# Kernel tuning notes

Hardware: AMD Instinct MI355X
Metric: run time of the kernel (lower is better)

The kernel has to match this reference:

```python
import jax, jax.numpy as jnp
import numpy as np

VOCAB = 10000
EMB = 512
CNN_FEAT = 2048
HID = 512
LAYERS = 2
BATCH = 128
SEQ = 32


def setup_inputs() -> dict:
    key = jax.random.key(0)
    ks = jax.random.split(key, 20)
    scale0 = 1.0 / np.sqrt(HID + EMB)
    scale1 = 1.0 / np.sqrt(HID + HID)
    inp = {
        "cnn_features": jax.random.normal(ks[0], (BATCH, CNN_FEAT), dtype=jnp.float32),
        "xTokens": jax.random.randint(ks[1], (BATCH, SEQ), 0, VOCAB),
        "embedding": jax.random.normal(ks[2], (VOCAB, EMB), dtype=jnp.float32),
        "in_W": jax.random.normal(ks[3], (CNN_FEAT, HID), dtype=jnp.float32) / np.sqrt(CNN_FEAT),
        "in_b": jnp.zeros((HID,), dtype=jnp.float32),
        # GRU layer 0 (input size EMB)
        "Wu0": jax.random.normal(ks[4], (EMB + HID, HID), dtype=jnp.float32) * scale0,
        "bu0": jnp.zeros((HID,), dtype=jnp.float32),
        "Wr0": jax.random.normal(ks[5], (EMB + HID, HID), dtype=jnp.float32) * scale0,
        "br0": jnp.zeros((HID,), dtype=jnp.float32),
        "Wc0": jax.random.normal(ks[6], (EMB + HID, HID), dtype=jnp.float32) * scale0,
        "bc0": jnp.zeros((HID,), dtype=jnp.float32),
        # GRU layer 1 (input size HID)
        "Wu1": jax.random.normal(ks[7], (HID + HID, HID), dtype=jnp.float32) * scale1,
        "bu1": jnp.zeros((HID,), dtype=jnp.float32),
        "Wr1": jax.random.normal(ks[8], (HID + HID, HID), dtype=jnp.float32) * scale1,
        "br1": jnp.zeros((HID,), dtype=jnp.float32),
        "Wc1": jax.random.normal(ks[9], (HID + HID, HID), dtype=jnp.float32) * scale1,
        "bc1": jnp.zeros((HID,), dtype=jnp.float32),
        "out_W": jax.random.normal(ks[10], (HID, VOCAB), dtype=jnp.float32) / np.sqrt(HID),
        "out_b": jnp.zeros((VOCAB,), dtype=jnp.float32),
    }
    return inp


def _gru(x, h, Wu, bu, Wr, br, Wc, bc):
    cat = jnp.concatenate([x, h], axis=1)                    # [B, in+H]
    u = jax.nn.sigmoid(cat @ Wu + bu)
    r = jax.nn.sigmoid(cat @ Wr + br)
    c = jnp.tanh(jnp.concatenate([x, r * h], axis=1) @ Wc + bc)
    return u * h + (1.0 - u) * c


def reference(cnn_features, xTokens, embedding, in_W, in_b,
              Wu0, bu0, Wr0, br0, Wc0, bc0,
              Wu1, bu1, Wr1, br1, Wc1, bc1,
              out_W, out_b):
    layer_params = [(Wu0, bu0, Wr0, br0, Wc0, bc0),
                    (Wu1, bu1, Wr1, br1, Wc1, bc1)]
    # initial hidden state from CNN features, replicated across layers
    h0 = jnp.tanh(cnn_features @ in_W + in_b)                # [B, H]
    init_state = jnp.broadcast_to(h0, (LAYERS,) + h0.shape)  # [L, B, H]
    emb = embedding[xTokens]                                 # [B, T, E]
    emb_t = jnp.transpose(emb, (1, 0, 2))                    # [T, B, E]

    def step(h, x_t):
        x = x_t
        new_h = []
        for j in range(LAYERS):
            x = _gru(x, h[j], *layer_params[j])
            new_h.append(x)
        logit = x @ out_W + out_b                            # [B, V]
        return jnp.stack(new_h, axis=0), logit

    final_state, logits_t = jax.lax.scan(step, init_state, emb_t)
    logits = jnp.transpose(logits_t, (1, 0, 2))              # [B, T, V]
    return logits, final_state
```

## Files before the change

### kernel.cpp

```cpp
#include <hip/hip_runtime.h>
#include <hip/hip_bf16.h>

#define BB 128
#define TT 32
#define HH 512
#define VV 10000
#define VPAD 10240
#define CFEAT 2048
#define MM 4096

typedef __attribute__((ext_vector_type(4))) float f32x4;
typedef __attribute__((ext_vector_type(8))) short short8v;
typedef __attribute__((ext_vector_type(4))) short short4v;

__device__ __forceinline__ void gload_lds16(const void* g, void* l) {
  __builtin_amdgcn_global_load_lds(
      (const __attribute__((address_space(1))) unsigned int*)g,
      (__attribute__((address_space(3))) unsigned int*)l, 16, 0, 0);
}

__device__ __forceinline__ float fsigmoid(float x) { return 1.0f / (1.0f + __expf(-x)); }
__device__ __forceinline__ float ftanh(float x) {
  x = fminf(15.0f, fmaxf(-15.0f, x));
  float t = __expf(2.0f * x);
  return (t - 1.0f) / (t + 1.0f);
}

__global__ __launch_bounds__(256)
void transpose_to_bf16(const float* __restrict__ in, int ldin, int K, int Nreal,
                       __hip_bfloat16* __restrict__ out)
{
  __shared__ float tile[32][33];
  const int tid = threadIdx.x;
  const int tx = tid & 31, ty = tid >> 5;
  const int k0 = blockIdx.y * 32;
  const int n0 = blockIdx.x * 32;
#pragma unroll
  for (int i = 0; i < 4; ++i) {
    int k = k0 + ty + i * 8;
    int n = n0 + tx;
    tile[ty + i * 8][tx] = (n < Nreal) ? in[(size_t)k * ldin + n] : 0.0f;
  }
  __syncthreads();
#pragma unroll
  for (int i = 0; i < 4; ++i) {
    int n = n0 + ty + i * 8;
    int k = k0 + tx;
    out[(size_t)n * K + k] = __float2bfloat16(tile[tx][ty + i * 8]);
  }
}

__global__ __launch_bounds__(256)
void h0_kernel(const float* __restrict__ cnn, const float* __restrict__ inW,
               const float* __restrict__ inb, float* __restrict__ h0,
               float* __restrict__ h1)
{
  __shared__ float xT[8][CFEAT];
  const int tid = threadIdx.x;
  const int r0 = blockIdx.y * 8;
  const int j0 = blockIdx.x * 64;
  {
    const float4* src = (const float4*)(cnn + (size_t)r0 * CFEAT);
    float4* dst = (float4*)&xT[0][0];
    for (int i = tid; i < 4096; i += 256) dst[i] = src[i];
  }
  __syncthreads();
  const int jj = tid & 63, rg = tid >> 6;
  const int j = j0 + jj;
  float a0 = 0.0f, a1 = 0.0f;
  for (int k4 = 0; k4 < CFEAT; k4 += 4) {
    f32x4 x0 = *(const f32x4*)&xT[rg * 2 + 0][k4];
    f32x4 x1 = *(const f32x4*)&xT[rg * 2 + 1][k4];
#pragma unroll
    for (int kk = 0; kk < 4; ++kk) {
      float wv = inW[(size_t)(k4 + kk) * HH + j];
      a0 += x0[kk] * wv;
      a1 += x1[kk] * wv;
    }
  }
  const float bb = inb[j];
  const int row0 = r0 + rg * 2;
  float v0 = ftanh(a0 + bb), v1 = ftanh(a1 + bb);
  h0[(size_t)(row0 + 0) * HH + j] = v0;  h1[(size_t)(row0 + 0) * HH + j] = v0;
  h0[(size_t)(row0 + 1) * HH + j] = v1;  h1[(size_t)(row0 + 1) * HH + j] = v1;
}

__global__ __launch_bounds__(128)
void gather_kernel(const int* __restrict__ xTok, const float* __restrict__ emb,
                   __hip_bfloat16* __restrict__ Xe)
{
  const int r = blockIdx.x;
  const int t = r >> 7, b = r & 127;
  const int tok = xTok[b * TT + t];
  float4 v = ((const float4*)(emb + (size_t)tok * HH))[threadIdx.x];
  __hip_bfloat16 o[4] = { __float2bfloat16(v.x), __float2bfloat16(v.y),
                          __float2bfloat16(v.z), __float2bfloat16(v.w) };
  *(short4v*)(Xe + (size_t)r * HH + threadIdx.x * 4) = *(const short4v*)o;
}

template<bool REMAP>
__global__ __launch_bounds__(256)
void mfma_gemm_bt(const __hip_bfloat16* __restrict__ A,
                  const __hip_bfloat16* __restrict__ BT,
                  const float* __restrict__ bias,
                  float* __restrict__ C, int Nreal)
{
  constexpr int K = 512;
  __shared__ __hip_bfloat16 ldsA[128 * 32];
  __shared__ __hip_bfloat16 ldsB[128 * 32];
  const int tid = threadIdx.x;
  const int lane = tid & 63;
  const int w = tid >> 6;
  const long m0 = (long)blockIdx.y * 128;
  const long n0 = (long)blockIdx.x * 128;
  const int wr = (w >> 1) * 64, wc = (w & 1) * 64;
  const int srow = lane >> 2;
  const int skoff = (lane & 3) * 8;
  f32x4 acc[4][4] = {};

  for (int kt = 0; kt < K; kt += 32) {
    __syncthreads();
#pragma unroll
    for (int i = 0; i < 2; ++i) {
      int c = w + i * 4;
      int row = c * 16 + srow;
      gload_lds16(A + (m0 + row) * K + kt + skoff, ldsA + c * 512 + lane * 8);
      gload_lds16(BT + (n0 + row) * K + kt + skoff, ldsB + c * 512 + lane * 8);
    }
    __syncthreads();
    short8v af[4], bfv[4];
#pragma unroll
    for (int m = 0; m < 4; ++m)
      af[m] = *(const short8v*)(ldsA + (wr + m * 16 + (lane & 15)) * 32 + (lane >> 4) * 8);
#pragma unroll
    for (int n = 0; n < 4; ++n)
      bfv[n] = *(const short8v*)(ldsB + (wc + n * 16 + (lane & 15)) * 32 + (lane >> 4) * 8);
#pragma unroll
    for (int m = 0; m < 4; ++m)
#pragma unroll
      for (int n = 0; n < 4; ++n)
        acc[m][n] = __builtin_amdgcn_mfma_f32_16x16x32_bf16(af[m], bfv[n], acc[m][n], 0, 0, 0);
  }

#pragma unroll
  for (int m = 0; m < 4; ++m) {
#pragma unroll
    for (int n = 0; n < 4; ++n) {
      int col = (int)n0 + wc + n * 16 + (lane & 15);
      if (col < Nreal) {
        float bv = bias[col];
#pragma unroll
        for (int q = 0; q < 4; ++q) {
          long row = m0 + wr + m * 16 + (lane >> 4) * 4 + q;
          float v = acc[m][n][q] + bv;
          if (REMAP) {
            long t = row >> 7, b = row & 127;
            C[(b * TT + t) * (long)Nreal + col] = v;
          } else {
            C[row * (long)Nreal + col] = v;
          }
        }
      }
    }
  }
}

__global__ __launch_bounds__(256)
void gru0_ur_kernel(const float* __restrict__ h,
                    const float* __restrict__ Wu, const float* __restrict__ Wr,
                    const float* __restrict__ preU, const float* __restrict__ preR,
                    float* __restrict__ u_out, float* __restrict__ rh_out, int t)
{
  __shared__ float hT[16][512];
  const int tid = threadIdx.x;
  const int r0 = blockIdx.y * 16;
  const int j0 = blockIdx.x * 64;
  const bool isU = (blockIdx.z == 0);
  const float* W = (isU ? Wu : Wr) + (size_t)HH * HH;
  const float* pre = isU ? preU : preR;
  {
    const float4* src = (const float4*)(h + (size_t)r0 * HH);
    float4* dst = (float4*)&hT[0][0];
    for (int i = tid; i < 2048; i += 256) dst[i] = src[i];
  }
  __syncthreads();
  const int jj = tid & 63, rg = tid >> 6;
  const int j = j0 + jj;
  f32x4 acc = {0.0f, 0.0f, 0.0f, 0.0f};
  for (int k4 = 0; k4 < 512; k4 += 4) {
    f32x4 h0v = *(const f32x4*)&hT[rg * 4 + 0][k4];
    f32x4 h1v = *(const f32x4*)&hT[rg * 4 + 1][k4];
    f32x4 h2v = *(const f32x4*)&hT[rg * 4 + 2][k4];
    f32x4 h3v = *(const f32x4*)&hT[rg * 4 + 3][k4];
#pragma unroll
    for (int kk = 0; kk < 4; ++kk) {
      float wv = W[(size_t)(k4 + kk) * HH + j];
      acc[0] += h0v[kk] * wv; acc[1] += h1v[kk] * wv;
      acc[2] += h2v[kk] * wv; acc[3] += h3v[kk] * wv;
    }
  }
#pragma unroll
  for (int q = 0; q < 4; ++q) {
    int row = r0 + rg * 4 + q;
    float pa = pre[(size_t)(t * BB + row) * HH + j];
    float s = fsigmoid(acc[q] + pa);
    if (isU) u_out[(size_t)row * HH + j] = s;
    else     rh_out[(size_t)row * HH + j] = s * hT[rg * 4 + q][j];
  }
}

__global__ __launch_bounds__(256)
void gru0_ch_kernel(float* __restrict__ h,
                    const float* __restrict__ Wc, const float* __restrict__ preC,
                    const float* __restrict__ u_in, const float* __restrict__ rh_in,
                    int t)
{
  __shared__ float rT[16][512];
  const int tid = threadIdx.x;
  const int r0 = blockIdx.y * 16;
  const int j0 = blockIdx.x * 64;
  const float* W = Wc + (size_t)HH * HH;
  {
    const float4* src = (const float4*)(rh_in + (size_t)r0 * HH);
    float4* dst = (float4*)&rT[0][0];
    for (int i = tid; i < 2048; i += 256) dst[i] = src[i];
  }
  __syncthreads();
  const int jj = tid & 63, rg = tid >> 6;
  const int j = j0 + jj;
  f32x4 acc = {0.0f, 0.0f, 0.0f, 0.0f};
  for (int k4 = 0; k4 < 512; k4 += 4) {
    f32x4 r0v = *(const f32x4*)&rT[rg * 4 + 0][k4];
    f32x4 r1v = *(const f32x4*)&rT[rg * 4 + 1][k4];
    f32x4 r2v = *(const f32x4*)&rT[rg * 4 + 2][k4];
    f32x4 r3v = *(const f32x4*)&rT[rg * 4 + 3][k4];
#pragma unroll
    for (int kk = 0; kk < 4; ++kk) {
      float wv = W[(size_t)(k4 + kk) * HH + j];
      acc[0] += r0v[kk] * wv; acc[1] += r1v[kk] * wv;
      acc[2] += r2v[kk] * wv; acc[3] += r3v[kk] * wv;
    }
  }
#pragma unroll
  for (int q = 0; q < 4; ++q) {
    int row = r0 + rg * 4 + q;
    size_t idx = (size_t)row * HH + j;
    float c = ftanh(acc[q] + preC[(size_t)(t * BB + row) * HH + j]);
    float u = u_in[idx];
    float hv = h[idx];
    h[idx] = u * hv + (1.0f - u) * c;
  }
}

__global__ __launch_bounds__(256)
void gru1_ur_kernel(const float* __restrict__ x, const float* __restrict__ h,
                    const float* __restrict__ Wu, const float* __restrict__ Wr,
                    const float* __restrict__ bu, const float* __restrict__ br,
                    float* __restrict__ u_out, float* __restrict__ rh_out)
{
  __shared__ float catT[16][1024];
  const int tid = threadIdx.x;
  const int r0 = blockIdx.y * 16;
  const int j0 = blockIdx.x * 64;
  const bool isU = (blockIdx.z == 0);
  const float* W = isU ? Wu : Wr;
  const float* bias = isU ? bu : br;
  {
    const float4* xs = (const float4*)(x + (size_t)r0 * HH);
    const float4* hs = (const float4*)(h + (size_t)r0 * HH);
    for (int i = tid; i < 2048; i += 256) {
      int r = i >> 7, c = i & 127;
      float4* rowp = (float4*)&catT[r][0];
      rowp[c] = xs[i];
      rowp[128 + c] = hs[i];
    }
  }
  __syncthreads();
  const int jj = tid & 63, rg = tid >> 6;
  const int j = j0 + jj;
  f32x4 acc = {0.0f, 0.0f, 0.0f, 0.0f};
  for (int k4 = 0; k4 < 1024; k4 += 4) {
    f32x4 c0v = *(const f32x4*)&catT[rg * 4 + 0][k4];
    f32x4 c1v = *(const f32x4*)&catT[rg * 4 + 1][k4];
    f32x4 c2v = *(const f32x4*)&catT[rg * 4 + 2][k4];
    f32x4 c3v = *(const f32x4*)&catT[rg * 4 + 3][k4];
#pragma unroll
    for (int kk = 0; kk < 4; ++kk) {
      float wv = W[(size_t)(k4 + kk) * HH + j];
      acc[0] += c0v[kk] * wv; acc[1] += c1v[kk] * wv;
      acc[2] += c2v[kk] * wv; acc[3] += c3v[kk] * wv;
    }
  }
  const float bb = bias[j];
#pragma unroll
  for (int q = 0; q < 4; ++q) {
    int row = r0 + rg * 4 + q;
    float s = fsigmoid(acc[q] + bb);
    if (isU) u_out[(size_t)row * HH + j] = s;
    else     rh_out[(size_t)row * HH + j] = s * catT[rg * 4 + q][512 + j];
  }
}

__global__ __launch_bounds__(256)
void gru1_ch_kernel(const float* __restrict__ x, float* __restrict__ h,
                    const float* __restrict__ Wc, const float* __restrict__ bc,
                    const float* __restrict__ u_in, const float* __restrict__ rh_in,
                    __hip_bfloat16* __restrict__ H1b, int t)
{
  __shared__ float catT[16][1024];
  const int tid = threadIdx.x;
  const int r0 = blockIdx.y * 16;
  const int j0 = blockIdx.x * 64;
  {
    const float4* xs = (const float4*)(x + (size_t)r0 * HH);
    const float4* rs = (const float4*)(rh_in + (size_t)r0 * HH);
    for (int i = tid; i < 2048; i += 256) {
      int r = i >> 7, c = i & 127;
      float4* rowp = (float4*)&catT[r][0];
      rowp[c] = xs[i];
      rowp[128 + c] = rs[i];
    }
  }
  __syncthreads();
  const int jj = tid & 63, rg = tid >> 6;
  const int j = j0 + jj;
  f32x4 acc = {0.0f, 0.0f, 0.0f, 0.0f};
  for (int k4 = 0; k4 < 1024; k4 += 4) {
    f32x4 c0v = *(const f32x4*)&catT[rg * 4 + 0][k4];
    f32x4 c1v = *(const f32x4*)&catT[rg * 4 + 1][k4];
    f32x4 c2v = *(const f32x4*)&catT[rg * 4 + 2][k4];
    f32x4 c3v = *(const f32x4*)&catT[rg * 4 + 3][k4];
#pragma unroll
    for (int kk = 0; kk < 4; ++kk) {
      float wv = Wc[(size_t)(k4 + kk) * HH + j];
      acc[0] += c0v[kk] * wv; acc[1] += c1v[kk] * wv;
      acc[2] += c2v[kk] * wv; acc[3] += c3v[kk] * wv;
    }
  }
  const float bb = bc[j];
#pragma unroll
  for (int q = 0; q < 4; ++q) {
    int row = r0 + rg * 4 + q;
    size_t idx = (size_t)row * HH + j;
    float c = ftanh(acc[q] + bb);
    float u = u_in[idx];
    float hv = h[idx];
    float hn = u * hv + (1.0f - u) * c;
    h[idx] = hn;
    H1b[(size_t)(t * BB + row) * HH + j] = __float2bfloat16(hn);
  }
}

__global__ __launch_bounds__(256)
void final_copy_kernel(const float* __restrict__ h0, const float* __restrict__ h1,
                       float* __restrict__ out)
{
  int i = blockIdx.x * 256 + threadIdx.x;
  out[(size_t)BB * TT * VV + i] = (i < BB * HH) ? h0[i] : h1[i - BB * HH];
}

extern "C" void kernel_launch(void* const* d_in, const int* in_sizes, int n_in,
                              void* d_out, int out_size, void* d_ws, size_t ws_size,
                              hipStream_t stream)
{
  (void)in_sizes; (void)n_in; (void)out_size; (void)ws_size;
  const float* cnn  = (const float*)d_in[0];
  const int*   xTok = (const int*)d_in[1];
  const float* emb  = (const float*)d_in[2];
  const float* inW  = (const float*)d_in[3];
  const float* inb  = (const float*)d_in[4];
  const float* Wu0  = (const float*)d_in[5];
  const float* bu0  = (const float*)d_in[6];
  const float* Wr0  = (const float*)d_in[7];
  const float* br0  = (const float*)d_in[8];
  const float* Wc0  = (const float*)d_in[9];
  const float* bc0  = (const float*)d_in[10];
  const float* Wu1  = (const float*)d_in[11];
  const float* bu1  = (const float*)d_in[12];
  const float* Wr1  = (const float*)d_in[13];
  const float* br1  = (const float*)d_in[14];
  const float* Wc1  = (const float*)d_in[15];
  const float* bc1  = (const float*)d_in[16];
  const float* outW = (const float*)d_in[17];
  const float* outb = (const float*)d_in[18];
  float* out = (float*)d_out;

  char* ws = (char*)d_ws;
  size_t off = 0;
  auto alloc = [&](size_t bytes) { void* p = ws + off; off += (bytes + 255) & ~(size_t)255; return p; };
  __hip_bfloat16* WoT = (__hip_bfloat16*)alloc((size_t)VPAD * HH * 2);
  __hip_bfloat16* WTu = (__hip_bfloat16*)alloc((size_t)HH * HH * 2);
  __hip_bfloat16* WTr = (__hip_bfloat16*)alloc((size_t)HH * HH * 2);
  __hip_bfloat16* WTc = (__hip_bfloat16*)alloc((size_t)HH * HH * 2);
  __hip_bfloat16* Xe  = (__hip_bfloat16*)alloc((size_t)MM * HH * 2);
  __hip_bfloat16* H1b = (__hip_bfloat16*)alloc((size_t)MM * HH * 2);
  float* h0s  = (float*)alloc((size_t)BB * HH * 4);
  float* h1s  = (float*)alloc((size_t)BB * HH * 4);
  float* u0b  = (float*)alloc((size_t)BB * HH * 4);
  float* rh0b = (float*)alloc((size_t)BB * HH * 4);
  float* u1b  = (float*)alloc((size_t)BB * HH * 4);
  float* rh1b = (float*)alloc((size_t)BB * HH * 4);
  float* preU = out;
  float* preR = out + (size_t)MM * HH;
  float* preC = out + (size_t)2 * MM * HH;

  transpose_to_bf16<<<dim3(VPAD / 32, HH / 32), 256, 0, stream>>>(outW, VV, HH, VV, WoT);
  transpose_to_bf16<<<dim3(HH / 32, HH / 32), 256, 0, stream>>>(Wu0, HH, HH, HH, WTu);
  transpose_to_bf16<<<dim3(HH / 32, HH / 32), 256, 0, stream>>>(Wr0, HH, HH, HH, WTr);
  transpose_to_bf16<<<dim3(HH / 32, HH / 32), 256, 0, stream>>>(Wc0, HH, HH, HH, WTc);

  h0_kernel<<<dim3(8, 16), 256, 0, stream>>>(cnn, inW, inb, h0s, h1s);

  gather_kernel<<<MM, 128, 0, stream>>>(xTok, emb, Xe);

  mfma_gemm_bt<false><<<dim3(HH / 128, MM / 128), 256, 0, stream>>>(Xe, WTu, bu0, preU, HH);
  mfma_gemm_bt<false><<<dim3(HH / 128, MM / 128), 256, 0, stream>>>(Xe, WTr, br0, preR, HH);
  mfma_gemm_bt<false><<<dim3(HH / 128, MM / 128), 256, 0, stream>>>(Xe, WTc, bc0, preC, HH);

  for (int t = 0; t < TT; ++t) {
    gru0_ur_kernel<<<dim3(8, 8, 2), 256, 0, stream>>>(h0s, Wu0, Wr0, preU, preR, u0b, rh0b, t);
    gru0_ch_kernel<<<dim3(8, 8), 256, 0, stream>>>(h0s, Wc0, preC, u0b, rh0b, t);
    gru1_ur_kernel<<<dim3(8, 8, 2), 256, 0, stream>>>(h0s, h1s, Wu1, Wr1, bu1, br1, u1b, rh1b);
    gru1_ch_kernel<<<dim3(8, 8), 256, 0, stream>>>(h0s, h1s, Wc1, bc1, u1b, rh1b, H1b, t);
  }

  mfma_gemm_bt<true><<<dim3(VPAD / 128, MM / 128), 256, 0, stream>>>(H1b, WoT, outb, out, VV);

  final_copy_kernel<<<512, 256, 0, stream>>>(h0s, h1s, out);
}
```

Measured before the change: 3.814 ms.

## Fuse the whole GRU time loop into one persistent MFMA scan kernel

Replaces 128 per-timestep fp32 FMA launches with a single persistent kernel of 8 blocks. Each block owns 16 batch rows, keeps both hidden states in LDS and runs all recurrent matmuls with bf16 MFMA against pre-transposed weights streamed from global/L2. The three layer-0 input projections are merged into one GEMM with N=1536, and the final state is written directly. This removes launch overhead and global round trips of intermediates. In exchange it uses only 8 CUs, rereads weights from L2 every step, and rounds the recurrent operands to bf16.

```diff
diff --git a/kernel.cpp b/kernel.cpp
--- a/kernel.cpp
+++ b/kernel.cpp
@@ -52,8 +52,7 @@
 
 __global__ __launch_bounds__(256)
 void h0_kernel(const float* __restrict__ cnn, const float* __restrict__ inW,
-               const float* __restrict__ inb, float* __restrict__ h0,
-               float* __restrict__ h1)
+               const float* __restrict__ inb, float* __restrict__ h0)
 {
   __shared__ float xT[8][CFEAT];
   const int tid = threadIdx.x;
@@ -80,9 +79,8 @@
   }
   const float bb = inb[j];
   const int row0 = r0 + rg * 2;
-  float v0 = ftanh(a0 + bb), v1 = ftanh(a1 + bb);
-  h0[(size_t)(row0 + 0) * HH + j] = v0;  h1[(size_t)(row0 + 0) * HH + j] = v0;
-  h0[(size_t)(row0 + 1) * HH + j] = v1;  h1[(size_t)(row0 + 1) * HH + j] = v1;
+  h0[(size_t)(row0 + 0) * HH + j] = ftanh(a0 + bb);
+  h0[(size_t)(row0 + 1) * HH + j] = ftanh(a1 + bb);
 }
 
 __global__ __launch_bounds__(128)
@@ -98,7 +96,7 @@
   *(short4v*)(Xe + (size_t)r * HH + threadIdx.x * 4) = *(const short4v*)o;
 }
 
-template<bool REMAP>
+template<bool REMAP, bool HASBIAS>
 __global__ __launch_bounds__(256)
 void mfma_gemm_bt(const __hip_bfloat16* __restrict__ A,
                   const __hip_bfloat16* __restrict__ BT,
@@ -148,7 +146,8 @@
     for (int n = 0; n < 4; ++n) {
       int col = (int)n0 + wc + n * 16 + (lane & 15);
       if (col < Nreal) {
-        float bv = bias[col];
+        float bv = 0.0f;
+        if constexpr (HASBIAS) bv = bias[col];
 #pragma unroll
         for (int q = 0; q < 4; ++q) {
           long row = m0 + wr + m * 16 + (lane >> 4) * 4 + q;
@@ -165,198 +164,163 @@
   }
 }
 
-__global__ __launch_bounds__(256)
-void gru0_ur_kernel(const float* __restrict__ h,
-                    const float* __restrict__ Wu, const float* __restrict__ Wr,
-                    const float* __restrict__ preU, const float* __restrict__ preR,
-                    float* __restrict__ u_out, float* __restrict__ rh_out, int t)
-{
-  __shared__ float hT[16][512];
+__device__ __forceinline__ void load_af(short8v af[16], const __hip_bfloat16* A,
+                                        int cl, int kh)
+{
+#pragma unroll
+  for (int kk = 0; kk < 16; ++kk)
+    af[kk] = *(const short8v*)(A + cl * 512 + kk * 32 + kh);
+}
+
+__device__ __forceinline__ void mm4(f32x4 acc[4], const short8v af[16],
+                                    const __hip_bfloat16* __restrict__ Wb,
+                                    int ldk, int col0, int cl, int kh)
+{
+#pragma unroll
+  for (int ct = 0; ct < 4; ++ct) {
+    const __hip_bfloat16* bp = Wb + (size_t)(col0 + ct * 16 + cl) * ldk + kh;
+    short8v bf[16];
+#pragma unroll
+    for (int kk = 0; kk < 16; ++kk) bf[kk] = *(const short8v*)(bp + kk * 32);
+#pragma unroll
+    for (int kk = 0; kk < 16; ++kk)
+      acc[ct] = __builtin_amdgcn_mfma_f32_16x16x32_bf16(af[kk], bf[kk], acc[ct], 0, 0, 0);
+  }
+}
+
+__global__ __launch_bounds__(512, 2)
+void gru_scan_kernel(const float* __restrict__ h0init,
+                     const float* __restrict__ pre,
+                     const __hip_bfloat16* __restrict__ WH0,
+                     const __hip_bfloat16* __restrict__ WT1,
+                     const float* __restrict__ bu0, const float* __restrict__ br0,
+                     const float* __restrict__ bc0,
+                     const float* __restrict__ bu1, const float* __restrict__ br1,
+                     const float* __restrict__ bc1,
+                     __hip_bfloat16* __restrict__ H1b,
+                     float* __restrict__ fstate)
+{
+  __shared__ float h0f[16 * 512];
+  __shared__ float h1f[16 * 512];
+  __shared__ __hip_bfloat16 Ab[2][16 * 512];
   const int tid = threadIdx.x;
-  const int r0 = blockIdx.y * 16;
-  const int j0 = blockIdx.x * 64;
-  const bool isU = (blockIdx.z == 0);
-  const float* W = (isU ? Wu : Wr) + (size_t)HH * HH;
-  const float* pre = isU ? preU : preR;
-  {
-    const float4* src = (const float4*)(h + (size_t)r0 * HH);
-    float4* dst = (float4*)&hT[0][0];
-    for (int i = tid; i < 2048; i += 256) dst[i] = src[i];
+  const int lane = tid & 63;
+  const int w = tid >> 6;
+  const int r0g = blockIdx.x * 16;
+  const int cl = lane & 15;
+  const int qh = lane >> 4;
+  const int kh = qh * 8;
+  const int wc0 = w * 64;
+
+  for (int i = tid; i < 16 * 512 / 4; i += 512) {
+    float4 v = ((const float4*)(h0init + (size_t)r0g * 512))[i];
+    ((float4*)h0f)[i] = v;
+    ((float4*)h1f)[i] = v;
+    __hip_bfloat16 o[4] = { __float2bfloat16(v.x), __float2bfloat16(v.y),
+                            __float2bfloat16(v.z), __float2bfloat16(v.w) };
+    short4v ov = *(const short4v*)o;
+    ((short4v*)Ab[0])[i] = ov;
+    ((short4v*)Ab[1])[i] = ov;
+  }
+  float bu0v[4], br0v[4], bc0v[4], bu1v[4], br1v[4], bc1v[4];
+#pragma unroll
+  for (int ct = 0; ct < 4; ++ct) {
+    int c = wc0 + ct * 16 + cl;
+    bu0v[ct] = bu0[c]; br0v[ct] = br0[c]; bc0v[ct] = bc0[c];
+    bu1v[ct] = bu1[c]; br1v[ct] = br1[c]; bc1v[ct] = bc1[c];
   }
   __syncthreads();
-  const int jj = tid & 63, rg = tid >> 6;
-  const int j = j0 + jj;
-  f32x4 acc = {0.0f, 0.0f, 0.0f, 0.0f};
-  for (int k4 = 0; k4 < 512; k4 += 4) {
-    f32x4 h0v = *(const f32x4*)&hT[rg * 4 + 0][k4];
-    f32x4 h1v = *(const f32x4*)&hT[rg * 4 + 1][k4];
-    f32x4 h2v = *(const f32x4*)&hT[rg * 4 + 2][k4];
-    f32x4 h3v = *(const f32x4*)&hT[rg * 4 + 3][k4];
-#pragma unroll
-    for (int kk = 0; kk < 4; ++kk) {
-      float wv = W[(size_t)(k4 + kk) * HH + j];
-      acc[0] += h0v[kk] * wv; acc[1] += h1v[kk] * wv;
-      acc[2] += h2v[kk] * wv; acc[3] += h3v[kk] * wv;
-    }
-  }
-#pragma unroll
-  for (int q = 0; q < 4; ++q) {
-    int row = r0 + rg * 4 + q;
-    float pa = pre[(size_t)(t * BB + row) * HH + j];
-    float s = fsigmoid(acc[q] + pa);
-    if (isU) u_out[(size_t)row * HH + j] = s;
-    else     rh_out[(size_t)row * HH + j] = s * hT[rg * 4 + q][j];
-  }
-}
-
-__global__ __launch_bounds__(256)
-void gru0_ch_kernel(float* __restrict__ h,
-                    const float* __restrict__ Wc, const float* __restrict__ preC,
-                    const float* __restrict__ u_in, const float* __restrict__ rh_in,
-                    int t)
-{
-  __shared__ float rT[16][512];
-  const int tid = threadIdx.x;
-  const int r0 = blockIdx.y * 16;
-  const int j0 = blockIdx.x * 64;
-  const float* W = Wc + (size_t)HH * HH;
-  {
-    const float4* src = (const float4*)(rh_in + (size_t)r0 * HH);
-    float4* dst = (float4*)&rT[0][0];
-    for (int i = tid; i < 2048; i += 256) dst[i] = src[i];
-  }
-  __syncthreads();
-  const int jj = tid & 63, rg = tid >> 6;
-  const int j = j0 + jj;
-  f32x4 acc = {0.0f, 0.0f, 0.0f, 0.0f};
-  for (int k4 = 0; k4 < 512; k4 += 4) {
-    f32x4 r0v = *(const f32x4*)&rT[rg * 4 + 0][k4];
-    f32x4 r1v = *(const f32x4*)&rT[rg * 4 + 1][k4];
-    f32x4 r2v = *(const f32x4*)&rT[rg * 4 + 2][k4];
-    f32x4 r3v = *(const f32x4*)&rT[rg * 4 + 3][k4];
-#pragma unroll
-    for (int kk = 0; kk < 4; ++kk) {
-      float wv = W[(size_t)(k4 + kk) * HH + j];
-      acc[0] += r0v[kk] * wv; acc[1] += r1v[kk] * wv;
-      acc[2] += r2v[kk] * wv; acc[3] += r3v[kk] * wv;
-    }
-  }
-#pragma unroll
-  for (int q = 0; q < 4; ++q) {
-    int row = r0 + rg * 4 + q;
-    size_t idx = (size_t)row * HH + j;
-    float c = ftanh(acc[q] + preC[(size_t)(t * BB + row) * HH + j]);
-    float u = u_in[idx];
-    float hv = h[idx];
-    h[idx] = u * hv + (1.0f - u) * c;
-  }
-}
-
-__global__ __launch_bounds__(256)
-void gru1_ur_kernel(const float* __restrict__ x, const float* __restrict__ h,
-                    const float* __restrict__ Wu, const float* __restrict__ Wr,
-                    const float* __restrict__ bu, const float* __restrict__ br,
-                    float* __restrict__ u_out, float* __restrict__ rh_out)
-{
-  __shared__ float catT[16][1024];
-  const int tid = threadIdx.x;
-  const int r0 = blockIdx.y * 16;
-  const int j0 = blockIdx.x * 64;
-  const bool isU = (blockIdx.z == 0);
-  const float* W = isU ? Wu : Wr;
-  const float* bias = isU ? bu : br;
-  {
-    const float4* xs = (const float4*)(x + (size_t)r0 * HH);
-    const float4* hs = (const float4*)(h + (size_t)r0 * HH);
-    for (int i = tid; i < 2048; i += 256) {
-      int r = i >> 7, c = i & 127;
-      float4* rowp = (float4*)&catT[r][0];
-      rowp[c] = xs[i];
-      rowp[128 + c] = hs[i];
-    }
-  }
-  __syncthreads();
-  const int jj = tid & 63, rg = tid >> 6;
-  const int j = j0 + jj;
-  f32x4 acc = {0.0f, 0.0f, 0.0f, 0.0f};
-  for (int k4 = 0; k4 < 1024; k4 += 4) {
-    f32x4 c0v = *(const f32x4*)&catT[rg * 4 + 0][k4];
-    f32x4 c1v = *(const f32x4*)&catT[rg * 4 + 1][k4];
-    f32x4 c2v = *(const f32x4*)&catT[rg * 4 + 2][k4];
-    f32x4 c3v = *(const f32x4*)&catT[rg * 4 + 3][k4];
-#pragma unroll
-    for (int kk = 0; kk < 4; ++kk) {
-      float wv = W[(size_t)(k4 + kk) * HH + j];
-      acc[0] += c0v[kk] * wv; acc[1] += c1v[kk] * wv;
-      acc[2] += c2v[kk] * wv; acc[3] += c3v[kk] * wv;
-    }
-  }
-  const float bb = bias[j];
-#pragma unroll
-  for (int q = 0; q < 4; ++q) {
-    int row = r0 + rg * 4 + q;
-    float s = fsigmoid(acc[q] + bb);
-    if (isU) u_out[(size_t)row * HH + j] = s;
-    else     rh_out[(size_t)row * HH + j] = s * catT[rg * 4 + q][512 + j];
-  }
-}
-
-__global__ __launch_bounds__(256)
-void gru1_ch_kernel(const float* __restrict__ x, float* __restrict__ h,
-                    const float* __restrict__ Wc, const float* __restrict__ bc,
-                    const float* __restrict__ u_in, const float* __restrict__ rh_in,
-                    __hip_bfloat16* __restrict__ H1b, int t)
-{
-  __shared__ float catT[16][1024];
-  const int tid = threadIdx.x;
-  const int r0 = blockIdx.y * 16;
-  const int j0 = blockIdx.x * 64;
-  {
-    const float4* xs = (const float4*)(x + (size_t)r0 * HH);
-    const float4* rs = (const float4*)(rh_in + (size_t)r0 * HH);
-    for (int i = tid; i < 2048; i += 256) {
-      int r = i >> 7, c = i & 127;
-      float4* rowp = (float4*)&catT[r][0];
-      rowp[c] = xs[i];
-      rowp[128 + c] = rs[i];
-    }
-  }
-  __syncthreads();
-  const int jj = tid & 63, rg = tid >> 6;
-  const int j = j0 + jj;
-  f32x4 acc = {0.0f, 0.0f, 0.0f, 0.0f};
-  for (int k4 = 0; k4 < 1024; k4 += 4) {
-    f32x4 c0v = *(const f32x4*)&catT[rg * 4 + 0][k4];
-    f32x4 c1v = *(const f32x4*)&catT[rg * 4 + 1][k4];
-    f32x4 c2v = *(const f32x4*)&catT[rg * 4 + 2][k4];
-    f32x4 c3v = *(const f32x4*)&catT[rg * 4 + 3][k4];
-#pragma unroll
-    for (int kk = 0; kk < 4; ++kk) {
-      float wv = Wc[(size_t)(k4 + kk) * HH + j];
-      acc[0] += c0v[kk] * wv; acc[1] += c1v[kk] * wv;
-      acc[2] += c2v[kk] * wv; acc[3] += c3v[kk] * wv;
-    }
-  }
-  const float bb = bc[j];
-#pragma unroll
-  for (int q = 0; q < 4; ++q) {
-    int row = r0 + rg * 4 + q;
-    size_t idx = (size_t)row * HH + j;
-    float c = ftanh(acc[q] + bb);
-    float u = u_in[idx];
-    float hv = h[idx];
-    float hn = u * hv + (1.0f - u) * c;
-    h[idx] = hn;
-    H1b[(size_t)(t * BB + row) * HH + j] = __float2bfloat16(hn);
-  }
-}
-
-__global__ __launch_bounds__(256)
-void final_copy_kernel(const float* __restrict__ h0, const float* __restrict__ h1,
-                       float* __restrict__ out)
-{
-  int i = blockIdx.x * 256 + threadIdx.x;
-  out[(size_t)BB * TT * VV + i] = (i < BB * HH) ? h0[i] : h1[i - BB * HH];
+
+  int p = 0;
+  for (int t = 0; t < TT; ++t) {
+    short8v af[16];
+    f32x4 u0a[4] = {}, r0a[4] = {}, u1a[4] = {}, r1a[4] = {};
+    load_af(af, Ab[p], cl, kh);
+    mm4(u0a, af, WH0, 512, wc0, cl, kh);
+    mm4(r0a, af, WH0 + (size_t)512 * 512, 512, wc0, cl, kh);
+    load_af(af, Ab[p ^ 1], cl, kh);
+    mm4(u1a, af, WT1 + 512, 1024, wc0, cl, kh);
+    mm4(r1a, af, WT1 + (size_t)512 * 1024 + 512, 1024, wc0, cl, kh);
+    __syncthreads();
+
+    float u0v[4][4], u1v[4][4];
+#pragma unroll
+    for (int ct = 0; ct < 4; ++ct) {
+      int c = wc0 + ct * 16 + cl;
+#pragma unroll
+      for (int q = 0; q < 4; ++q) {
+        int r = qh * 4 + q;
+        size_t prow = (size_t)(t * BB + r0g + r) * 1536;
+        float u0 = fsigmoid(u0a[ct][q] + bu0v[ct] + pre[prow + c]);
+        float r0 = fsigmoid(r0a[ct][q] + br0v[ct] + pre[prow + 512 + c]);
+        u0v[ct][q] = u0;
+        Ab[p][r * 512 + c] = __float2bfloat16(r0 * h0f[r * 512 + c]);
+      }
+    }
+    __syncthreads();
+    f32x4 c0a[4] = {};
+    load_af(af, Ab[p], cl, kh);
+    mm4(c0a, af, WH0 + (size_t)1024 * 512, 512, wc0, cl, kh);
+#pragma unroll
+    for (int ct = 0; ct < 4; ++ct) {
+      int c = wc0 + ct * 16 + cl;
+#pragma unroll
+      for (int q = 0; q < 4; ++q) {
+        int r = qh * 4 + q;
+        size_t prow = (size_t)(t * BB + r0g + r) * 1536;
+        float c0 = ftanh(c0a[ct][q] + bc0v[ct] + pre[prow + 1024 + c]);
+        float ho = h0f[r * 512 + c];
+        float hn = u0v[ct][q] * ho + (1.0f - u0v[ct][q]) * c0;
+        h0f[r * 512 + c] = hn;
+        Ab[p ^ 1][r * 512 + c] = __float2bfloat16(hn);
+      }
+    }
+    __syncthreads();
+    f32x4 c1a[4] = {};
+    load_af(af, Ab[p ^ 1], cl, kh);
+    mm4(u1a, af, WT1, 1024, wc0, cl, kh);
+    mm4(r1a, af, WT1 + (size_t)512 * 1024, 1024, wc0, cl, kh);
+    mm4(c1a, af, WT1 + (size_t)1024 * 1024, 1024, wc0, cl, kh);
+#pragma unroll
+    for (int ct = 0; ct < 4; ++ct) {
+      int c = wc0 + ct * 16 + cl;
+#pragma unroll
+      for (int q = 0; q < 4; ++q) {
+        int r = qh * 4 + q;
+        float u1 = fsigmoid(u1a[ct][q] + bu1v[ct]);
+        float r1 = fsigmoid(r1a[ct][q] + br1v[ct]);
+        u1v[ct][q] = u1;
+        Ab[p][r * 512 + c] = __float2bfloat16(r1 * h1f[r * 512 + c]);
+      }
+    }
+    __syncthreads();
+    load_af(af, Ab[p], cl, kh);
+    mm4(c1a, af, WT1 + (size_t)1024 * 1024 + 512, 1024, wc0, cl, kh);
+    __syncthreads();
+#pragma unroll
+    for (int ct = 0; ct < 4; ++ct) {
+      int c = wc0 + ct * 16 + cl;
+#pragma unroll
+      for (int q = 0; q < 4; ++q) {
+        int r = qh * 4 + q;
+        float c1 = ftanh(c1a[ct][q] + bc1v[ct]);
+        float h1o = h1f[r * 512 + c];
+        float hn = u1v[ct][q] * h1o + (1.0f - u1v[ct][q]) * c1;
+        h1f[r * 512 + c] = hn;
+        __hip_bfloat16 hb = __float2bfloat16(hn);
+        Ab[p][r * 512 + c] = hb;
+        H1b[(size_t)(t * BB + r0g + r) * 512 + c] = hb;
+      }
+    }
+    __syncthreads();
+    p ^= 1;
+  }
+
+  for (int i = tid; i < 16 * 512; i += 512) {
+    int r = i >> 9, c = i & 511;
+    fstate[(size_t)(r0g + r) * 512 + c] = h0f[i];
+    fstate[(size_t)BB * 512 + (size_t)(r0g + r) * 512 + c] = h1f[i];
+  }
 }
 
 extern "C" void kernel_launch(void* const* d_in, const int* in_sizes, int n_in,
@@ -388,43 +352,35 @@
   char* ws = (char*)d_ws;
   size_t off = 0;
   auto alloc = [&](size_t bytes) { void* p = ws + off; off += (bytes + 255) & ~(size_t)255; return p; };
-  __hip_bfloat16* WoT = (__hip_bfloat16*)alloc((size_t)VPAD * HH * 2);
-  __hip_bfloat16* WTu = (__hip_bfloat16*)alloc((size_t)HH * HH * 2);
-  __hip_bfloat16* WTr = (__hip_bfloat16*)alloc((size_t)HH * HH * 2);
-  __hip_bfloat16* WTc = (__hip_bfloat16*)alloc((size_t)HH * HH * 2);
-  __hip_bfloat16* Xe  = (__hip_bfloat16*)alloc((size_t)MM * HH * 2);
-  __hip_bfloat16* H1b = (__hip_bfloat16*)alloc((size_t)MM * HH * 2);
-  float* h0s  = (float*)alloc((size_t)BB * HH * 4);
-  float* h1s  = (float*)alloc((size_t)BB * HH * 4);
-  float* u0b  = (float*)alloc((size_t)BB * HH * 4);
-  float* rh0b = (float*)alloc((size_t)BB * HH * 4);
-  float* u1b  = (float*)alloc((size_t)BB * HH * 4);
-  float* rh1b = (float*)alloc((size_t)BB * HH * 4);
-  float* preU = out;
-  float* preR = out + (size_t)MM * HH;
-  float* preC = out + (size_t)2 * MM * HH;
+  __hip_bfloat16* WoT   = (__hip_bfloat16*)alloc((size_t)VPAD * HH * 2);
+  __hip_bfloat16* WXcat = (__hip_bfloat16*)alloc((size_t)3 * HH * HH * 2);
+  __hip_bfloat16* WH0   = (__hip_bfloat16*)alloc((size_t)3 * HH * HH * 2);
+  __hip_bfloat16* WT1   = (__hip_bfloat16*)alloc((size_t)3 * HH * 2 * HH * 2);
+  __hip_bfloat16* Xe    = (__hip_bfloat16*)alloc((size_t)MM * HH * 2);
+  __hip_bfloat16* H1b   = (__hip_bfloat16*)alloc((size_t)MM * HH * 2);
+  float* h0s = (float*)alloc((size_t)BB * HH * 4);
+  float* pre = out;
 
   transpose_to_bf16<<<dim3(VPAD / 32, HH / 32), 256, 0, stream>>>(outW, VV, HH, VV, WoT);
-  transpose_to_bf16<<<dim3(HH / 32, HH / 32), 256, 0, stream>>>(Wu0, HH, HH, HH, WTu);
-  transpose_to_bf16<<<dim3(HH / 32, HH / 32), 256, 0, stream>>>(Wr0, HH, HH, HH, WTr);
-  transpose_to_bf16<<<dim3(HH / 32, HH / 32), 256, 0, stream>>>(Wc0, HH, HH, HH, WTc);
-
-  h0_kernel<<<dim3(8, 16), 256, 0, stream>>>(cnn, inW, inb, h0s, h1s);
+  transpose_to_bf16<<<dim3(16, 16), 256, 0, stream>>>(Wu0, HH, HH, HH, WXcat);
+  transpose_to_bf16<<<dim3(16, 16), 256, 0, stream>>>(Wr0, HH, HH, HH, WXcat + (size_t)HH * HH);
+  transpose_to_bf16<<<dim3(16, 16), 256, 0, stream>>>(Wc0, HH, HH, HH, WXcat + (size_t)2 * HH * HH);
+  transpose_to_bf16<<<dim3(16, 16), 256, 0, stream>>>(Wu0 + (size_t)HH * HH, HH, HH, HH, WH0);
+  transpose_to_bf16<<<dim3(16, 16), 256, 0, stream>>>(Wr0 + (size_t)HH * HH, HH, HH, HH, WH0 + (size_t)HH * HH);
+  transpose_to_bf16<<<dim3(16, 16), 256, 0, stream>>>(Wc0 + (size_t)HH * HH, HH, HH, HH, WH0 + (size_t)2 * HH * HH);
+  transpose_to_bf16<<<dim3(16, 32), 256, 0, stream>>>(Wu1, HH, 2 * HH, HH, WT1);
+  transpose_to_bf16<<<dim3(16, 32), 256, 0, stream>>>(Wr1, HH, 2 * HH, HH, WT1 + (size_t)HH * 2 * HH);
+  transpose_to_bf16<<<dim3(16, 32), 256, 0, stream>>>(Wc1, HH, 2 * HH, HH, WT1 + (size_t)2 * HH * 2 * HH);
+
+  h0_kernel<<<dim3(8, 16), 256, 0, stream>>>(cnn, inW, inb, h0s);
 
   gather_kernel<<<MM, 128, 0, stream>>>(xTok, emb, Xe);
 
-  mfma_gemm_bt<false><<<dim3(HH / 128, MM / 128), 256, 0, stream>>>(Xe, WTu, bu0, preU, HH);
-  mfma_gemm_bt<false><<<dim3(HH / 128, MM / 128), 256, 0, stream>>>(Xe, WTr, br0, preR, HH);
-  mfma_gemm_bt<false><<<dim3(HH / 128, MM / 128), 256, 0, stream>>>(Xe, WTc, bc0, preC, HH);
-
-  for (int t = 0; t < TT; ++t) {
-    gru0_ur_kernel<<<dim3(8, 8, 2), 256, 0, stream>>>(h0s, Wu0, Wr0, preU, preR, u0b, rh0b, t);
-    gru0_ch_kernel<<<dim3(8, 8), 256, 0, stream>>>(h0s, Wc0, preC, u0b, rh0b, t);
-    gru1_ur_kernel<<<dim3(8, 8, 2), 256, 0, stream>>>(h0s, h1s, Wu1, Wr1, bu1, br1, u1b, rh1b);
-    gru1_ch_kernel<<<dim3(8, 8), 256, 0, stream>>>(h0s, h1s, Wc1, bc1, u1b, rh1b, H1b, t);
-  }
-
-  mfma_gemm_bt<true><<<dim3(VPAD / 128, MM / 128), 256, 0, stream>>>(H1b, WoT, outb, out, VV);
-
-  final_copy_kernel<<<512, 256, 0, stream>>>(h0s, h1s, out);
-}
+  mfma_gemm_bt<false, false><<<dim3(12, MM / 128), 256, 0, stream>>>(Xe, WXcat, nullptr, pre, 1536);
+
+  gru_scan_kernel<<<8, 512, 0, stream>>>(h0s, pre, WH0, WT1,
+                                         bu0, br0, bc0, bu1, br1, bc1,
+                                         H1b, out + (size_t)MM * VV);
+
+  mfma_gemm_bt<true, true><<<dim3(VPAD / 128, MM / 128), 256, 0, stream>>>(H1b, WoT, outb, out, VV);
+}
```

Result: slower. 6.374 ms (+67.1%).
